# Performance work log

Hardware: AMD Instinct MI355X
Metric: run time of the kernel (lower is better)

Reference implementation:

```python
import jax, jax.numpy as jnp
import numpy as np

DIM = 16            # Hilbert space dimension
D = DIM * DIM       # superoperator / vectorized-density dimension (256)
N_TS = 128          # number of timesteps
N_CTRLS = 2         # number of control fields
DT = 0.02           # timestep
SQUARINGS = 6       # scaling-and-squaring steps for matrix_exp
TAYLOR_TERMS = 12   # Taylor (Horner) order for matrix_exp


def setup_inputs() -> dict:
    key = jax.random.key(0)
    ks = jax.random.split(key, 12)
    s = 0.05  # keep generator norms small so expm(A*dt) is well-conditioned
    D2 = (D, D)
    ctrls_real = jax.random.normal(ks[0], (N_TS, N_CTRLS), jnp.float32)
    ctrls_im = jax.random.normal(ks[1], (N_TS, N_CTRLS), jnp.float32)
    dyn_gen_re = s * jax.random.normal(ks[2], D2, jnp.float32)
    dyn_gen_im = s * jax.random.normal(ks[3], D2, jnp.float32)
    ctrl_gen_re = s * jax.random.normal(ks[4], (N_CTRLS, 2, D, D), jnp.float32)
    ctrl_gen_im = s * jax.random.normal(ks[5], (N_CTRLS, 2, D, D), jnp.float32)
    # initial / target: vectorized density-like states (identity/DIM + noise)
    eye_vec = (jnp.eye(DIM, dtype=jnp.float32) / DIM).reshape(D)
    initial_re = eye_vec + 0.01 * jax.random.normal(ks[6], (D,), jnp.float32)
    initial_im = 0.01 * jax.random.normal(ks[7], (D,), jnp.float32)
    target_re = eye_vec + 0.01 * jax.random.normal(ks[8], (D,), jnp.float32)
    target_im = 0.01 * jax.random.normal(ks[9], (D,), jnp.float32)
    return dict(ctrls_real=ctrls_real, ctrls_im=ctrls_im,
                dyn_gen_re=dyn_gen_re, dyn_gen_im=dyn_gen_im,
                ctrl_gen_re=ctrl_gen_re, ctrl_gen_im=ctrl_gen_im,
                initial_re=initial_re, initial_im=initial_im,
                target_re=target_re, target_im=target_im)


def _expm(A):
    """Differentiable matrix exponential: scaling-and-squaring + Taylor (Horner)."""
    A = A / (2.0 ** SQUARINGS)
    I = jnp.eye(A.shape[-1], dtype=A.dtype)
    R = I
    for k in range(TAYLOR_TERMS, 0, -1):
        R = I + (A @ R) / k
    for _ in range(SQUARINGS):
        R = R @ R
    return R


def _evolve(cr, ci, dyn, Gr, Gi, s0):
    # control generators: _get_ctrl_gen -> cr*(G0+G1) + 1j*ci*(G0-G1)
    G0 = Gr[:, 0] + 1j * Gi[:, 0]   # [n_ctrls, D, D]
    G1 = Gr[:, 1] + 1j * Gi[:, 1]
    Gp = G0 + G1
    Gm = G0 - G1
    crc = cr.astype(Gp.dtype)
    cic = ci.astype(Gm.dtype)
    # per-timestep dynamics generator A_k = dyn + sum_j ctrl terms  [n_ts, D, D]
    A = (dyn[None, :, :]
         + jnp.einsum('kj,jab->kab', crc, Gp)
         + 1j * jnp.einsum('kj,jab->kab', cic, Gm))
    props = jax.vmap(_expm)(A * DT)  # [n_ts, D, D]
    diag_idx = jnp.arange(DIM) * (DIM + 1)  # trace indices of vec(rho)

    def step(s, P):
        s = P @ s
        s = s / s[diag_idx].sum()  # trace normalization
        return s, None

    sT, _ = jax.lax.scan(step, s0, props)
    return sT


def reference(ctrls_real, ctrls_im, dyn_gen_re, dyn_gen_im,
              ctrl_gen_re, ctrl_gen_im, initial_re, initial_im,
              target_re, target_im):
    dyn = dyn_gen_re + 1j * dyn_gen_im
    s0 = initial_re + 1j * initial_im
    sT = _evolve(ctrls_real, ctrls_im, dyn, ctrl_gen_re, ctrl_gen_im, s0)
    tgt = target_re + 1j * target_im
    fid_err = jnp.linalg.norm((sT - tgt).reshape(DIM, DIM))  # Frobenius norm
    return sT, fid_err
```

## Files before the change

kernel.cpp:

```cpp
#include <hip/hip_runtime.h>
#include <math.h>

#define DD    256
#define PLQ   65536
#define SLOTB 131072
#define NTS   128
#define DT_C  0.02f

typedef unsigned short u16;
typedef unsigned int   u32;
typedef __attribute__((ext_vector_type(8))) short s16x8;
typedef __attribute__((ext_vector_type(4))) float f32x4;

typedef __attribute__((address_space(1))) const unsigned int GU32;
typedef __attribute__((address_space(3))) unsigned int LU32;

__device__ __forceinline__ u32 swzB(u32 b) {
    return b ^ (((((b >> 7) ^ (b >> 10)) & 7u)) << 4);
}
__device__ __forceinline__ u16 f2bf(float f) {
    u32 u = __float_as_uint(f);
    return (u16)((u + 0x7FFFu + ((u >> 16) & 1u)) >> 16);
}
__device__ __forceinline__ float bf2f(u16 h) {
    return __uint_as_float(((u32)h) << 16);
}
__device__ __forceinline__ void gll16(const u16* g, char* ldsBase, u32 ldsByteOff) {
    u32 off = (u32)__builtin_amdgcn_readfirstlane((int)ldsByteOff);
    __builtin_amdgcn_global_load_lds((GU32*)g, (LU32*)(ldsBase + off), 16, 0, 0);
}

__global__ __launch_bounds__(256)
void build_kernel(const float* __restrict__ cr, const float* __restrict__ ci,
                  const float* __restrict__ dre, const float* __restrict__ dimg,
                  const float* __restrict__ gre, const float* __restrict__ gim,
                  u16* __restrict__ Xn, int ts0)
{
    const int ts = blockIdx.y;
    const int k  = ts0 + ts;
    const int i4 = (blockIdx.x * 256 + threadIdx.x) * 4;

    const float c0f = cr[2*k], c1f = cr[2*k+1];
    const float e0f = ci[2*k], e1f = ci[2*k+1];

    const float4 g0r = *(const float4*)&gre[0*PLQ + i4];
    const float4 g1r = *(const float4*)&gre[1*PLQ + i4];
    const float4 g2r = *(const float4*)&gre[2*PLQ + i4];
    const float4 g3r = *(const float4*)&gre[3*PLQ + i4];
    const float4 g0i = *(const float4*)&gim[0*PLQ + i4];
    const float4 g1i = *(const float4*)&gim[1*PLQ + i4];
    const float4 g2i = *(const float4*)&gim[2*PLQ + i4];
    const float4 g3i = *(const float4*)&gim[3*PLQ + i4];
    const float4 d_r = *(const float4*)&dre[i4];
    const float4 d_i = *(const float4*)&dimg[i4];
    const float* gr00 = &g0r.x; const float* gr01 = &g1r.x;
    const float* gr10 = &g2r.x; const float* gr11 = &g3r.x;
    const float* gi00 = &g0i.x; const float* gi01 = &g1i.x;
    const float* gi10 = &g2i.x; const float* gi11 = &g3i.x;
    const float* dr4  = &d_r.x; const float* di4  = &d_i.x;

    ushort4 hr, hi;
    u16* hrp = &hr.x; u16* hip = &hi.x;
    #pragma unroll
    for (int j = 0; j < 4; ++j) {
        const float are = dr4[j] + c0f*(gr00[j]+gr01[j]) + c1f*(gr10[j]+gr11[j])
                                 - e0f*(gi00[j]-gi01[j]) - e1f*(gi10[j]-gi11[j]);
        const float aim = di4[j] + c0f*(gi00[j]+gi01[j]) + c1f*(gi10[j]+gi11[j])
                                 + e0f*(gr00[j]-gr01[j]) + e1f*(gr10[j]-gr11[j]);
        hrp[j] = f2bf(DT_C * are);
        hip[j] = f2bf(DT_C * aim);
    }
    u16* X = Xn + (size_t)ts * SLOTB;
    *(ushort4*)&X[i4]       = hr;
    *(ushort4*)&X[PLQ + i4] = hi;
}

template<int TRB>
__global__ __launch_bounds__(256)
void cgemm(const u16* __restrict__ Ab, const u16* __restrict__ Bb,
           u16* __restrict__ outN,
           const u16* __restrict__ X1b, const u16* __restrict__ X2b,
           float aN, float bN1, float bN2,
           int aS, int aO, int bS, int bO, int cS, int cO,
           int x1S, int x1O, int x2S, int x2O)
{
    __shared__ char lds[32768];

    const u32 nwg = 16u * (u32)gridDim.z;
    const u32 wg  = (u32)blockIdx.x + 4u*(u32)blockIdx.y + 16u*(u32)blockIdx.z;
    const u32 q   = nwg >> 3;
    const u32 w   = (wg & 7u) * q + (wg >> 3);
    const int bn = (int)(w & 3u) * 64;
    const int bm = (int)((w >> 2) & 3u) * 64;
    const int z  = (int)(w >> 4);

    const u16* __restrict__ A = Ab + (size_t)(z*aS + aO) * SLOTB;
    const u16* __restrict__ B = Bb + (size_t)(z*bS + bO) * SLOTB;

    const int t = threadIdx.x;

    const u32 b0 = (u32)t * 16u, b1 = 4096u + (u32)t * 16u;
    const u32 L0 = swzB(b0),     L1 = swzB(b1);
    const int rA0 = (int)(L0 >> 7), kA0 = (int)((L0 & 127u) >> 1);
    const int rA1 = (int)(L1 >> 7), kA1 = (int)((L1 & 127u) >> 1);
    const u32 wvoff = ((u32)(t >> 6)) * 1024u;

    const u16* pA0 = A + (size_t)(bm + rA0)*DD + kA0;
    const u16* pA1 = A + (size_t)(bm + rA1)*DD + kA1;

    const int kRow = t >> 3;
    const int nCh  = t & 7;

    const int wv = t >> 6, ln = t & 63;
    const int wrow = (wv >> 1) * 32, wcol = (wv & 1) * 32;
    const int lg = ln >> 4, lc = ln & 15;

    f32x4 accR[2][2], accI[2][2];
    #pragma unroll
    for (int i = 0; i < 2; ++i)
        #pragma unroll
        for (int j = 0; j < 2; ++j) {
            accR[i][j] = (f32x4){0.f,0.f,0.f,0.f};
            accI[i][j] = (f32x4){0.f,0.f,0.f,0.f};
        }

    {
        gll16(pA0,       lds, wvoff +     0u);
        gll16(pA1,       lds, wvoff +  4096u);
        gll16(pA0 + PLQ, lds, wvoff +  8192u);
        gll16(pA1 + PLQ, lds, wvoff + 12288u);
        #pragma unroll
        for (int h = 0; h < 2; ++h) {
            const int kk = h*32 + kRow;
            const s16x8 vr = *(const s16x8*)(B +       (size_t)kk*DD + bn + nCh*8);
            const s16x8 vi = *(const s16x8*)(B + PLQ + (size_t)kk*DD + bn + nCh*8);
            #pragma unroll
            for (int e = 0; e < 8; ++e) {
                const u32 off = swzB((u32)(nCh*8 + e)*128u + (u32)kk*2u);
                *(u16*)(lds + 16384 + off) = (u16)vr[e];
                *(u16*)(lds + 24576 + off) = (u16)vi[e];
            }
        }
    }
    __syncthreads();

    for (int it = 0; it < 4; ++it) {
        s16x8 nvr0, nvi0, nvr1, nvi1;
        if (it < 3) {
            const int k1 = 64*(it + 1);
            nvr0 = *(const s16x8*)(B +       (size_t)(k1 + kRow)*DD + bn + nCh*8);
            nvi0 = *(const s16x8*)(B + PLQ + (size_t)(k1 + kRow)*DD + bn + nCh*8);
            nvr1 = *(const s16x8*)(B +       (size_t)(k1 + 32 + kRow)*DD + bn + nCh*8);
            nvi1 = *(const s16x8*)(B + PLQ + (size_t)(k1 + 32 + kRow)*DD + bn + nCh*8);
        }

        #pragma unroll
        for (int s = 0; s < 2; ++s) {
            s16x8 ar[2], ai[2], br[2], bi[2];
            #pragma unroll
            for (int fm = 0; fm < 2; ++fm) {
                const u32 so = swzB((u32)(wrow + fm*16 + lc)*128u + (u32)(s*4 + lg)*16u);
                ar[fm] = *(const s16x8*)(lds + so);
                ai[fm] = *(const s16x8*)(lds + 8192 + so);
            }
            #pragma unroll
            for (int fn = 0; fn < 2; ++fn) {
                const u32 so = swzB((u32)(wcol + fn*16 + lc)*128u + (u32)(s*4 + lg)*16u);
                br[fn] = *(const s16x8*)(lds + 16384 + so);
                bi[fn] = *(const s16x8*)(lds + 24576 + so);
            }
            #pragma unroll
            for (int fm = 0; fm < 2; ++fm)
                #pragma unroll
                for (int fn = 0; fn < 2; ++fn) {
                    accI[fm][fn] = __builtin_amdgcn_mfma_f32_16x16x32_bf16(ar[fm], bi[fn], accI[fm][fn], 0, 0, 0);
                    accI[fm][fn] = __builtin_amdgcn_mfma_f32_16x16x32_bf16(ai[fm], br[fn], accI[fm][fn], 0, 0, 0);
                }
            #pragma unroll
            for (int fm = 0; fm < 2; ++fm) ai[fm] ^= (short)0x8000u;
            #pragma unroll
            for (int fm = 0; fm < 2; ++fm)
                #pragma unroll
                for (int fn = 0; fn < 2; ++fn) {
                    accR[fm][fn] = __builtin_amdgcn_mfma_f32_16x16x32_bf16(ar[fm], br[fn], accR[fm][fn], 0, 0, 0);
                    accR[fm][fn] = __builtin_amdgcn_mfma_f32_16x16x32_bf16(ai[fm], bi[fn], accR[fm][fn], 0, 0, 0);
                }
        }

        if (it < 3) {
            const int k1 = 64*(it + 1);
            __syncthreads();
            gll16(pA0 + k1,       lds, wvoff +     0u);
            gll16(pA1 + k1,       lds, wvoff +  4096u);
            gll16(pA0 + PLQ + k1, lds, wvoff +  8192u);
            gll16(pA1 + PLQ + k1, lds, wvoff + 12288u);
            #pragma unroll
            for (int e = 0; e < 8; ++e) {
                const u32 off0 = swzB((u32)(nCh*8 + e)*128u + (u32)kRow*2u);
                const u32 off1 = swzB((u32)(nCh*8 + e)*128u + (u32)(32 + kRow)*2u);
                *(u16*)(lds + 16384 + off0) = (u16)nvr0[e];
                *(u16*)(lds + 24576 + off0) = (u16)nvi0[e];
                *(u16*)(lds + 16384 + off1) = (u16)nvr1[e];
                *(u16*)(lds + 24576 + off1) = (u16)nvi1[e];
            }
            __syncthreads();
        }
    }

    u16* oN = outN + (size_t)(z*cS + cO) * SLOTB;
    const u16* x1 = X1b ? X1b + (size_t)(z*x1S + x1O) * SLOTB : nullptr;
    const u16* x2 = X2b ? X2b + (size_t)(z*x2S + x2O) * SLOTB : nullptr;

    #pragma unroll
    for (int fm = 0; fm < 2; ++fm)
        #pragma unroll
        for (int fn = 0; fn < 2; ++fn) {
            const int rb = bm + wrow + fm*16 + lg*4;
            const int c  = bn + wcol + fn*16 + lc;
            #pragma unroll
            for (int j = 0; j < 4; ++j) {
                const int r = rb + j;
                float x1r = 0.f, x1i = 0.f, x2r = 0.f, x2i = 0.f;
                if (x1) { x1r = bf2f(x1[(size_t)r*DD + c]);
                          x1i = bf2f(x1[PLQ + (size_t)r*DD + c]); }
                if (x2) { x2r = bf2f(x2[(size_t)r*DD + c]);
                          x2i = bf2f(x2[PLQ + (size_t)r*DD + c]); }
                oN[(size_t)r*DD + c]       = f2bf(aN*accR[fm][fn][j] + bN1*x1r + bN2*x2r);
                oN[PLQ + (size_t)r*DD + c] = f2bf(aN*accI[fm][fn][j] + bN1*x1i + bN2*x2i);
            }
        }
}

__global__ __launch_bounds__(256)
void final_kernel(const u16* __restrict__ Et,
                  const float* __restrict__ s0r, const float* __restrict__ s0i,
                  const float* __restrict__ tgr, const float* __restrict__ tgi,
                  float* __restrict__ out, int outSize)
{
    __shared__ float sr[DD], si[DD], red[DD];
    __shared__ float cR, cI;
    const int t = threadIdx.x;
    sr[t] = s0r[t];
    si[t] = s0i[t];
    __syncthreads();

    const u16* Er = Et + (size_t)t*DD;
    const u16* Ei = Er + PLQ;
    float ar = sr[t], ai = si[t];
    for (int kk = 0; kk < DD/8; ++kk) {
        const s16x8 er = *(const s16x8*)(Er + kk*8);
        const s16x8 ei = *(const s16x8*)(Ei + kk*8);
        #pragma unroll
        for (int jj = 0; jj < 8; ++jj) {
            const float pr = bf2f((u16)er[jj]);
            const float pi = bf2f((u16)ei[jj]);
            const int k = kk*8 + jj;
            ar += pr*sr[k] - pi*si[k];
            ai += pr*si[k] + pi*sr[k];
        }
    }
    __syncthreads();
    sr[t] = ar; si[t] = ai;
    __syncthreads();

    if (t == 0) {
        float xr = 0.f, xi = 0.f;
        for (int i = 0; i < 16; ++i) { xr += sr[i*17]; xi += si[i*17]; }
        cR = xr; cI = xi;
    }
    __syncthreads();

    const float den = cR*cR + cI*cI;
    const float str = (ar*cR + ai*cI) / den;
    const float sti = (ai*cR - ar*cI) / den;

    const float dr = str - tgr[t];
    const float di = sti - tgi[t];
    red[t] = dr*dr + di*di;
    __syncthreads();
    for (int s = 128; s > 0; s >>= 1) {
        if (t < s) red[t] += red[t + s];
        __syncthreads();
    }
    const float fid = sqrtf(red[0]);

    if (outSize >= 2*DD + 1) {
        out[2*t] = str; out[2*t+1] = sti;
        if (t == 0) out[2*DD] = fid;
    } else if (outSize == 2*DD) {
        out[2*t] = str; out[2*t+1] = sti;
    } else {
        out[t] = str;
        if (t == 0 && outSize > DD) out[DD] = fid;
    }
}

extern "C" void kernel_launch(void* const* d_in, const int* in_sizes, int n_in,
                              void* d_out, int out_size, void* d_ws, size_t ws_size,
                              hipStream_t stream)
{
    (void)in_sizes; (void)n_in;
    const float* cr   = (const float*)d_in[0];
    const float* ci   = (const float*)d_in[1];
    const float* dre  = (const float*)d_in[2];
    const float* dimg = (const float*)d_in[3];
    const float* gre  = (const float*)d_in[4];
    const float* gim  = (const float*)d_in[5];
    const float* s0r  = (const float*)d_in[6];
    const float* s0i  = (const float*)d_in[7];
    const float* tgr  = (const float*)d_in[8];
    const float* tgi  = (const float*)d_in[9];

    const float c2 = 0.5f, c3i = 1.f/6.f;

    u16* ws = (u16*)d_ws;
    const long slots = (long)(ws_size / 2) / SLOTB;

    if (slots >= 384) {
        u16* RX = ws;
        u16* R1 = ws + 128L * SLOTB;
        u16* R2 = ws + 256L * SLOTB;

        build_kernel<<<dim3(PLQ/1024, 128), 256, 0, stream>>>(
            cr, ci, dre, dimg, gre, gim, RX, 0);

        const dim3 g128(4, 4, 128);
        cgemm<1><<<g128, 256, 0, stream>>>(RX, RX, R1, nullptr, nullptr,
            1.f, 0.f, 0.f,
            1,0, 1,0, 1,0, 0,0, 0,0);
        cgemm<1><<<g128, 256, 0, stream>>>(R1, RX, R2, RX, R1,
            c3i, 1.f, c2,
            1,0, 1,0, 1,0, 1,0, 1,0);

        u16* cur = R2;
        u16* oth = R1;
        for (int n = 128; n > 1; n >>= 1) {
            cgemm<1><<<dim3(4, 4, n/2), 256, 0, stream>>>(
                cur, cur, oth, cur, cur,
                1.f, 1.f, 1.f,
                2,1, 2,0, 1,0, 2,1, 2,0);
            u16* tmp = cur; cur = oth; oth = tmp;
        }
        final_kernel<<<1, 256, 0, stream>>>(cur, s0r, s0i, tgr, tgi,
                                            (float*)d_out, out_size);
    } else {
        u16* P  = ws;
        u16* CB = ws + 128L * SLOTB;
        int C = (int)((slots - 128) / 2);
        if (C > NTS) C = NTS;
        if (C < 32)  C = 32;

        for (int ts0 = 0; ts0 < NTS; ts0 += C) {
            int nb = NTS - ts0; if (nb > C) nb = C;
            u16* Xn = CB;
            u16* P2 = CB + 1L*C*SLOTB;

            build_kernel<<<dim3(PLQ/1024, nb), 256, 0, stream>>>(
                cr, ci, dre, dimg, gre, gim, Xn, ts0);

            const dim3 grid(4, 4, nb);
            cgemm<1><<<grid, 256, 0, stream>>>(Xn, Xn, P2, nullptr, nullptr,
                1.f, 0.f, 0.f,
                1,0, 1,0, 1,0, 0,0, 0,0);
            cgemm<1><<<grid, 256, 0, stream>>>(P2, Xn, P, Xn, P2,
                c3i, 1.f, c2,
                1,0, 1,0, 1,ts0, 1,0, 1,0);
        }

        u16* cur = P;
        u16* oth = CB;
        for (int n = 128; n > 1; n >>= 1) {
            cgemm<1><<<dim3(4, 4, n/2), 256, 0, stream>>>(
                cur, cur, oth, cur, cur,
                1.f, 1.f, 1.f,
                2,1, 2,0, 1,0, 2,1, 2,0);
            u16* tmp = cur; cur = oth; oth = tmp;
        }
        final_kernel<<<1, 256, 0, stream>>>(cur, s0r, s0i, tgr, tgi,
                                            (float*)d_out, out_size);
    }
}
```

Measured before the change: 214.7 us.

## Double-buffer LDS tiles in complex GEMM to overlap global loads with MFMA

Doubles the LDS allocation to two 32KB buffers and issues the next K-slice's direct-to-LDS A loads and B register loads before computing the current slice. Explicit vmcnt waits and raw s_barrier replace the two __syncthreads per iteration, and s_setprio raises wave priority during the MFMA section. This aims to hide global-memory latency behind compute, at the cost of 64KB LDS per block, which may reduce occupancy.

```diff
diff --git a/kernel.cpp b/kernel.cpp
--- a/kernel.cpp
+++ b/kernel.cpp
@@ -84,7 +84,7 @@
            int aS, int aO, int bS, int bO, int cS, int cO,
            int x1S, int x1O, int x2S, int x2O)
 {
-    __shared__ char lds[32768];
+    __shared__ char lds[65536];
 
     const u32 nwg = 16u * (u32)gridDim.z;
     const u32 wg  = (u32)blockIdx.x + 4u*(u32)blockIdx.y + 16u*(u32)blockIdx.z;
@@ -124,50 +124,64 @@
             accI[i][j] = (f32x4){0.f,0.f,0.f,0.f};
         }
 
+    s16x8 vr0, vi0, vr1, vi1;
     {
         gll16(pA0,       lds, wvoff +     0u);
         gll16(pA1,       lds, wvoff +  4096u);
         gll16(pA0 + PLQ, lds, wvoff +  8192u);
         gll16(pA1 + PLQ, lds, wvoff + 12288u);
-        #pragma unroll
-        for (int h = 0; h < 2; ++h) {
-            const int kk = h*32 + kRow;
-            const s16x8 vr = *(const s16x8*)(B +       (size_t)kk*DD + bn + nCh*8);
-            const s16x8 vi = *(const s16x8*)(B + PLQ + (size_t)kk*DD + bn + nCh*8);
-            #pragma unroll
-            for (int e = 0; e < 8; ++e) {
-                const u32 off = swzB((u32)(nCh*8 + e)*128u + (u32)kk*2u);
-                *(u16*)(lds + 16384 + off) = (u16)vr[e];
-                *(u16*)(lds + 24576 + off) = (u16)vi[e];
-            }
-        }
-    }
-    __syncthreads();
+        vr0 = *(const s16x8*)(B +       (size_t)kRow*DD + bn + nCh*8);
+        vi0 = *(const s16x8*)(B + PLQ + (size_t)kRow*DD + bn + nCh*8);
+        vr1 = *(const s16x8*)(B +       (size_t)(32 + kRow)*DD + bn + nCh*8);
+        vi1 = *(const s16x8*)(B + PLQ + (size_t)(32 + kRow)*DD + bn + nCh*8);
+    }
 
     for (int it = 0; it < 4; ++it) {
-        s16x8 nvr0, nvi0, nvr1, nvi1;
+        const u32 cb = (u32)(it & 1) * 32768u;
+        const u32 sb = cb ^ 32768u;
+        s16x8 nr0, ni0, nr1, ni1;
         if (it < 3) {
             const int k1 = 64*(it + 1);
-            nvr0 = *(const s16x8*)(B +       (size_t)(k1 + kRow)*DD + bn + nCh*8);
-            nvi0 = *(const s16x8*)(B + PLQ + (size_t)(k1 + kRow)*DD + bn + nCh*8);
-            nvr1 = *(const s16x8*)(B +       (size_t)(k1 + 32 + kRow)*DD + bn + nCh*8);
-            nvi1 = *(const s16x8*)(B + PLQ + (size_t)(k1 + 32 + kRow)*DD + bn + nCh*8);
-        }
-
+            gll16(pA0 + k1,       lds, sb + wvoff +     0u);
+            gll16(pA1 + k1,       lds, sb + wvoff +  4096u);
+            gll16(pA0 + PLQ + k1, lds, sb + wvoff +  8192u);
+            gll16(pA1 + PLQ + k1, lds, sb + wvoff + 12288u);
+            nr0 = *(const s16x8*)(B +       (size_t)(k1 + kRow)*DD + bn + nCh*8);
+            ni0 = *(const s16x8*)(B + PLQ + (size_t)(k1 + kRow)*DD + bn + nCh*8);
+            nr1 = *(const s16x8*)(B +       (size_t)(k1 + 32 + kRow)*DD + bn + nCh*8);
+            ni1 = *(const s16x8*)(B + PLQ + (size_t)(k1 + 32 + kRow)*DD + bn + nCh*8);
+            asm volatile("s_waitcnt vmcnt(8)" ::: "memory");
+        } else {
+            asm volatile("s_waitcnt vmcnt(0)" ::: "memory");
+        }
+        __builtin_amdgcn_sched_barrier(0);
+
+        #pragma unroll
+        for (int e = 0; e < 8; ++e) {
+            const u32 off0 = swzB((u32)(nCh*8 + e)*128u + (u32)kRow*2u);
+            const u32 off1 = swzB((u32)(nCh*8 + e)*128u + (u32)(32 + kRow)*2u);
+            *(u16*)(lds + cb + 16384 + off0) = (u16)vr0[e];
+            *(u16*)(lds + cb + 24576 + off0) = (u16)vi0[e];
+            *(u16*)(lds + cb + 16384 + off1) = (u16)vr1[e];
+            *(u16*)(lds + cb + 24576 + off1) = (u16)vi1[e];
+        }
+        asm volatile("s_waitcnt lgkmcnt(0)\n\ts_barrier" ::: "memory");
+
+        __builtin_amdgcn_s_setprio(1);
         #pragma unroll
         for (int s = 0; s < 2; ++s) {
             s16x8 ar[2], ai[2], br[2], bi[2];
             #pragma unroll
             for (int fm = 0; fm < 2; ++fm) {
                 const u32 so = swzB((u32)(wrow + fm*16 + lc)*128u + (u32)(s*4 + lg)*16u);
-                ar[fm] = *(const s16x8*)(lds + so);
-                ai[fm] = *(const s16x8*)(lds + 8192 + so);
+                ar[fm] = *(const s16x8*)(lds + cb + so);
+                ai[fm] = *(const s16x8*)(lds + cb + 8192 + so);
             }
             #pragma unroll
             for (int fn = 0; fn < 2; ++fn) {
                 const u32 so = swzB((u32)(wcol + fn*16 + lc)*128u + (u32)(s*4 + lg)*16u);
-                br[fn] = *(const s16x8*)(lds + 16384 + so);
-                bi[fn] = *(const s16x8*)(lds + 24576 + so);
+                br[fn] = *(const s16x8*)(lds + cb + 16384 + so);
+                bi[fn] = *(const s16x8*)(lds + cb + 24576 + so);
             }
             #pragma unroll
             for (int fm = 0; fm < 2; ++fm)
@@ -186,25 +200,11 @@
                     accR[fm][fn] = __builtin_amdgcn_mfma_f32_16x16x32_bf16(ai[fm], bi[fn], accR[fm][fn], 0, 0, 0);
                 }
         }
-
-        if (it < 3) {
-            const int k1 = 64*(it + 1);
-            __syncthreads();
-            gll16(pA0 + k1,       lds, wvoff +     0u);
-            gll16(pA1 + k1,       lds, wvoff +  4096u);
-            gll16(pA0 + PLQ + k1, lds, wvoff +  8192u);
-            gll16(pA1 + PLQ + k1, lds, wvoff + 12288u);
-            #pragma unroll
-            for (int e = 0; e < 8; ++e) {
-                const u32 off0 = swzB((u32)(nCh*8 + e)*128u + (u32)kRow*2u);
-                const u32 off1 = swzB((u32)(nCh*8 + e)*128u + (u32)(32 + kRow)*2u);
-                *(u16*)(lds + 16384 + off0) = (u16)nvr0[e];
-                *(u16*)(lds + 24576 + off0) = (u16)nvi0[e];
-                *(u16*)(lds + 16384 + off1) = (u16)nvr1[e];
-                *(u16*)(lds + 24576 + off1) = (u16)nvi1[e];
-            }
-            __syncthreads();
-        }
+        __builtin_amdgcn_s_setprio(0);
+
+        asm volatile("s_barrier" ::: "memory");
+
+        vr0 = nr0; vi0 = ni0; vr1 = nr1; vi1 = ni1;
     }
 
     u16* oN = outN + (size_t)(z*cS + cO) * SLOTB;
```

Result: slower. 221.0 us (+2.9%).

## Add 128x128-tile complex GEMM kernel and select by batch size

Applied to the files above, without the earlier changes.

Adds a new batched complex bf16 GEMM that uses 128x128 output tiles, a 64KB double-buffered LDS stage and a different swizzle. It is used for the expm Taylor GEMMs and for the large-batch levels of the product tree, while the existing 64x64 kernel is kept for levels with fewer than 32 products. Larger tiles should give more operand reuse per loaded byte and fewer workgroups. The cost is lower occupancy from the larger LDS footprint and more accumulator registers, plus fewer workgroups to fill the CUs.

```diff
diff --git a/kernel.cpp b/kernel.cpp
--- a/kernel.cpp
+++ b/kernel.cpp
@@ -17,6 +17,9 @@
 
 __device__ __forceinline__ u32 swzB(u32 b) {
     return b ^ (((((b >> 7) ^ (b >> 10)) & 7u)) << 4);
+}
+__device__ __forceinline__ u32 swzA(u32 b) {
+    return b ^ ((((b >> 6) ^ (b >> 8)) & 3u) << 4);
 }
 __device__ __forceinline__ u16 f2bf(float f) {
     u32 u = __float_as_uint(f);
@@ -75,14 +78,156 @@
     *(ushort4*)&X[PLQ + i4] = hi;
 }
 
-template<int TRB>
 __global__ __launch_bounds__(256)
-void cgemm(const u16* __restrict__ Ab, const u16* __restrict__ Bb,
-           u16* __restrict__ outN,
-           const u16* __restrict__ X1b, const u16* __restrict__ X2b,
-           float aN, float bN1, float bN2,
-           int aS, int aO, int bS, int bO, int cS, int cO,
-           int x1S, int x1O, int x2S, int x2O)
+void cgemm128(const u16* __restrict__ Ab, const u16* __restrict__ Bb,
+              u16* __restrict__ outN,
+              const u16* __restrict__ X1b, const u16* __restrict__ X2b,
+              float aN, float bN1, float bN2,
+              int aS, int aO, int bS, int bO, int cS, int cO,
+              int x1S, int x1O, int x2S, int x2O)
+{
+    __shared__ char lds[65536];
+
+    const u32 nwg = 4u * (u32)gridDim.z;
+    const u32 wg  = (u32)blockIdx.x + 2u*(u32)blockIdx.y + 4u*(u32)blockIdx.z;
+    u32 w = wg;
+    if ((nwg & 7u) == 0u) { const u32 q = nwg >> 3; w = (wg & 7u)*q + (wg >> 3); }
+    const int bn = (int)(w & 1u) * 128;
+    const int bm = (int)((w >> 1) & 1u) * 128;
+    const int z  = (int)(w >> 2);
+
+    const u16* __restrict__ A = Ab + (size_t)(z*aS + aO) * SLOTB;
+    const u16* __restrict__ B = Bb + (size_t)(z*bS + bO) * SLOTB;
+
+    const int t = threadIdx.x;
+
+    const u32 b0 = (u32)t * 16u, b1 = 4096u + (u32)t * 16u;
+    const u32 L0 = swzA(b0),     L1 = swzA(b1);
+    const int rA0 = (int)(L0 >> 6), kA0 = (int)((L0 & 63u) >> 1);
+    const int rA1 = (int)(L1 >> 6), kA1 = (int)((L1 & 63u) >> 1);
+    const u32 wvoff = ((u32)(t >> 6)) * 1024u;
+
+    const u16* pA0 = A + (size_t)(bm + rA0)*DD + kA0;
+    const u16* pA1 = A + (size_t)(bm + rA1)*DD + kA1;
+
+    const int kRow = t >> 4;
+    const int nCh  = t & 15;
+
+    const int wv = t >> 6, ln = t & 63;
+    const int wrow = (wv >> 1) * 64, wcol = (wv & 1) * 64;
+    const int lg = ln >> 4, lc = ln & 15;
+
+    f32x4 accR[4][4], accI[4][4];
+    #pragma unroll
+    for (int i = 0; i < 4; ++i)
+        #pragma unroll
+        for (int j = 0; j < 4; ++j) {
+            accR[i][j] = (f32x4){0.f,0.f,0.f,0.f};
+            accI[i][j] = (f32x4){0.f,0.f,0.f,0.f};
+        }
+
+    s16x8 vr0, vi0, vr1, vi1;
+    {
+        gll16(pA0,       lds, wvoff +     0u);
+        gll16(pA1,       lds, wvoff +  4096u);
+        gll16(pA0 + PLQ, lds, wvoff +  8192u);
+        gll16(pA1 + PLQ, lds, wvoff + 12288u);
+        vr0 = *(const s16x8*)(B +       (size_t)kRow*DD + bn + nCh*8);
+        vi0 = *(const s16x8*)(B + PLQ + (size_t)kRow*DD + bn + nCh*8);
+        vr1 = *(const s16x8*)(B +       (size_t)(16 + kRow)*DD + bn + nCh*8);
+        vi1 = *(const s16x8*)(B + PLQ + (size_t)(16 + kRow)*DD + bn + nCh*8);
+    }
+
+    for (int it = 0; it < 8; ++it) {
+        const u32 cb = (u32)(it & 1) * 32768u;
+        const u32 sb = cb ^ 32768u;
+        s16x8 nr0, ni0, nr1, ni1;
+        if (it < 7) {
+            const int k1 = 32*(it + 1);
+            gll16(pA0 + k1,       lds, sb + wvoff +     0u);
+            gll16(pA1 + k1,       lds, sb + wvoff +  4096u);
+            gll16(pA0 + PLQ + k1, lds, sb + wvoff +  8192u);
+            gll16(pA1 + PLQ + k1, lds, sb + wvoff + 12288u);
+            nr0 = *(const s16x8*)(B +       (size_t)(k1 + kRow)*DD + bn + nCh*8);
+            ni0 = *(const s16x8*)(B + PLQ + (size_t)(k1 + kRow)*DD + bn + nCh*8);
+            nr1 = *(const s16x8*)(B +       (size_t)(k1 + 16 + kRow)*DD + bn + nCh*8);
+            ni1 = *(const s16x8*)(B + PLQ + (size_t)(k1 + 16 + kRow)*DD + bn + nCh*8);
+            asm volatile("s_waitcnt vmcnt(8)" ::: "memory");
+        } else {
+            asm volatile("s_waitcnt vmcnt(0)" ::: "memory");
+        }
+        __builtin_amdgcn_sched_barrier(0);
+
+        #pragma unroll
+        for (int e = 0; e < 8; ++e) {
+            const u32 o0 = swzA((u32)(nCh*8 + e)*64u + (u32)kRow*2u);
+            const u32 o1 = swzA((u32)(nCh*8 + e)*64u + (u32)(16 + kRow)*2u);
+            *(u16*)(lds + cb + 16384 + o0) = (u16)vr0[e];
+            *(u16*)(lds + cb + 24576 + o0) = (u16)vi0[e];
+            *(u16*)(lds + cb + 16384 + o1) = (u16)vr1[e];
+            *(u16*)(lds + cb + 24576 + o1) = (u16)vi1[e];
+        }
+        asm volatile("s_waitcnt lgkmcnt(0)\n\ts_barrier" ::: "memory");
+
+        __builtin_amdgcn_s_setprio(1);
+        s16x8 br[4], bi[4];
+        #pragma unroll
+        for (int fn = 0; fn < 4; ++fn) {
+            const u32 so = swzA((u32)(wcol + fn*16 + lc)*64u + (u32)lg*16u);
+            br[fn] = *(const s16x8*)(lds + cb + 16384 + so);
+            bi[fn] = *(const s16x8*)(lds + cb + 24576 + so);
+        }
+        #pragma unroll
+        for (int fm = 0; fm < 4; ++fm) {
+            const u32 so = swzA((u32)(wrow + fm*16 + lc)*64u + (u32)lg*16u);
+            const s16x8 a_r = *(const s16x8*)(lds + cb + so);
+            const s16x8 a_i = *(const s16x8*)(lds + cb + 8192 + so);
+            const s16x8 a_n = a_i ^ (short)0x8000u;
+            #pragma unroll
+            for (int fn = 0; fn < 4; ++fn) {
+                accI[fm][fn] = __builtin_amdgcn_mfma_f32_16x16x32_bf16(a_r, bi[fn], accI[fm][fn], 0, 0, 0);
+                accI[fm][fn] = __builtin_amdgcn_mfma_f32_16x16x32_bf16(a_i, br[fn], accI[fm][fn], 0, 0, 0);
+                accR[fm][fn] = __builtin_amdgcn_mfma_f32_16x16x32_bf16(a_r, br[fn], accR[fm][fn], 0, 0, 0);
+                accR[fm][fn] = __builtin_amdgcn_mfma_f32_16x16x32_bf16(a_n, bi[fn], accR[fm][fn], 0, 0, 0);
+            }
+        }
+        __builtin_amdgcn_s_setprio(0);
+
+        asm volatile("s_barrier" ::: "memory");
+        vr0 = nr0; vi0 = ni0; vr1 = nr1; vi1 = ni1;
+    }
+
+    u16* oN = outN + (size_t)(z*cS + cO) * SLOTB;
+    const u16* x1 = X1b ? X1b + (size_t)(z*x1S + x1O) * SLOTB : nullptr;
+    const u16* x2 = X2b ? X2b + (size_t)(z*x2S + x2O) * SLOTB : nullptr;
+
+    #pragma unroll
+    for (int fm = 0; fm < 4; ++fm)
+        #pragma unroll
+        for (int fn = 0; fn < 4; ++fn) {
+            const int rb = bm + wrow + fm*16 + lg*4;
+            const int c  = bn + wcol + fn*16 + lc;
+            #pragma unroll
+            for (int j = 0; j < 4; ++j) {
+                const int r = rb + j;
+                float x1r = 0.f, x1i = 0.f, x2r = 0.f, x2i = 0.f;
+                if (x1) { x1r = bf2f(x1[(size_t)r*DD + c]);
+                          x1i = bf2f(x1[PLQ + (size_t)r*DD + c]); }
+                if (x2) { x2r = bf2f(x2[(size_t)r*DD + c]);
+                          x2i = bf2f(x2[PLQ + (size_t)r*DD + c]); }
+                oN[(size_t)r*DD + c]       = f2bf(aN*accR[fm][fn][j] + bN1*x1r + bN2*x2r);
+                oN[PLQ + (size_t)r*DD + c] = f2bf(aN*accI[fm][fn][j] + bN1*x1i + bN2*x2i);
+            }
+        }
+}
+
+__global__ __launch_bounds__(256)
+void cgemm64(const u16* __restrict__ Ab, const u16* __restrict__ Bb,
+             u16* __restrict__ outN,
+             const u16* __restrict__ X1b, const u16* __restrict__ X2b,
+             float aN, float bN1, float bN2,
+             int aS, int aO, int bS, int bO, int cS, int cO,
+             int x1S, int x1O, int x2S, int x2O)
 {
     __shared__ char lds[32768];
 
@@ -324,21 +469,28 @@
         build_kernel<<<dim3(PLQ/1024, 128), 256, 0, stream>>>(
             cr, ci, dre, dimg, gre, gim, RX, 0);
 
-        const dim3 g128(4, 4, 128);
-        cgemm<1><<<g128, 256, 0, stream>>>(RX, RX, R1, nullptr, nullptr,
+        cgemm128<<<dim3(2, 2, 128), 256, 0, stream>>>(RX, RX, R1, nullptr, nullptr,
             1.f, 0.f, 0.f,
             1,0, 1,0, 1,0, 0,0, 0,0);
-        cgemm<1><<<g128, 256, 0, stream>>>(R1, RX, R2, RX, R1,
+        cgemm128<<<dim3(2, 2, 128), 256, 0, stream>>>(R1, RX, R2, RX, R1,
             c3i, 1.f, c2,
             1,0, 1,0, 1,0, 1,0, 1,0);
 
         u16* cur = R2;
         u16* oth = R1;
         for (int n = 128; n > 1; n >>= 1) {
-            cgemm<1><<<dim3(4, 4, n/2), 256, 0, stream>>>(
-                cur, cur, oth, cur, cur,
-                1.f, 1.f, 1.f,
-                2,1, 2,0, 1,0, 2,1, 2,0);
+            const int hz = n/2;
+            if (hz >= 32) {
+                cgemm128<<<dim3(2, 2, hz), 256, 0, stream>>>(
+                    cur, cur, oth, cur, cur,
+                    1.f, 1.f, 1.f,
+                    2,1, 2,0, 1,0, 2,1, 2,0);
+            } else {
+                cgemm64<<<dim3(4, 4, hz), 256, 0, stream>>>(
+                    cur, cur, oth, cur, cur,
+                    1.f, 1.f, 1.f,
+                    2,1, 2,0, 1,0, 2,1, 2,0);
+            }
             u16* tmp = cur; cur = oth; oth = tmp;
         }
         final_kernel<<<1, 256, 0, stream>>>(cur, s0r, s0i, tgr, tgi,
@@ -358,11 +510,10 @@
             build_kernel<<<dim3(PLQ/1024, nb), 256, 0, stream>>>(
                 cr, ci, dre, dimg, gre, gim, Xn, ts0);
 
-            const dim3 grid(4, 4, nb);
-            cgemm<1><<<grid, 256, 0, stream>>>(Xn, Xn, P2, nullptr, nullptr,
+            cgemm128<<<dim3(2, 2, nb), 256, 0, stream>>>(Xn, Xn, P2, nullptr, nullptr,
                 1.f, 0.f, 0.f,
                 1,0, 1,0, 1,0, 0,0, 0,0);
-            cgemm<1><<<grid, 256, 0, stream>>>(P2, Xn, P, Xn, P2,
+            cgemm128<<<dim3(2, 2, nb), 256, 0, stream>>>(P2, Xn, P, Xn, P2,
                 c3i, 1.f, c2,
                 1,0, 1,0, 1,ts0, 1,0, 1,0);
         }
@@ -370,10 +521,18 @@
         u16* cur = P;
         u16* oth = CB;
         for (int n = 128; n > 1; n >>= 1) {
-            cgemm<1><<<dim3(4, 4, n/2), 256, 0, stream>>>(
-                cur, cur, oth, cur, cur,
-                1.f, 1.f, 1.f,
-                2,1, 2,0, 1,0, 2,1, 2,0);
+            const int hz = n/2;
+            if (hz >= 32) {
+                cgemm128<<<dim3(2, 2, hz), 256, 0, stream>>>(
+                    cur, cur, oth, cur, cur,
+                    1.f, 1.f, 1.f,
+                    2,1, 2,0, 1,0, 2,1, 2,0);
+            } else {
+                cgemm64<<<dim3(4, 4, hz), 256, 0, stream>>>(
+                    cur, cur, oth, cur, cur,
+                    1.f, 1.f, 1.f,
+                    2,1, 2,0, 1,0, 2,1, 2,0);
+            }
             u16* tmp = cur; cur = oth; oth = tmp;
         }
         final_kernel<<<1, 256, 0, stream>>>(cur, s0r, s0i, tgr, tgi,
```

After: 333.3 us. 55.2% more time.
